# Performance work log

Measured on AMD Instinct MI355X. Metric: run time of the kernel, lower is better.

## Reference

```python
import jax, jax.numpy as jnp
import numpy as np

NUM_HEADS = 16


def setup_inputs() -> dict:
    key = jax.random.key(0)
    ks = jax.random.split(key, 3)
    B, S, E = 8, 1024, 1024
    x = jax.random.normal(ks[0], (B, S, E), dtype=jnp.float32)
    W_attn = jax.random.normal(ks[1], (E, 3 * E), dtype=jnp.float32) * (1.0 / np.sqrt(E))
    b_attn = jnp.zeros((3 * E,), dtype=jnp.float32)
    W_proj = jax.random.normal(ks[2], (E, E), dtype=jnp.float32) * (1.0 / np.sqrt(E))
    b_proj = jnp.zeros((E,), dtype=jnp.float32)
    return {"x": x, "W_attn": W_attn, "b_attn": b_attn, "W_proj": W_proj, "b_proj": b_proj}


def reference(x, W_attn, b_attn, W_proj, b_proj):
    # The module's blockwise "flash" loop implements exact causal softmax
    # attention (online softmax is mathematically identical); dropout is
    # inactive in eval mode.
    B, S, E = x.shape
    H = NUM_HEADS
    D = E // H
    qkv = x @ W_attn + b_attn  # [B,S,3E]
    q, k, v = jnp.split(qkv, 3, axis=-1)

    def split_heads(t):
        return t.reshape(B, S, H, D).transpose(0, 2, 1, 3)  # [B,H,S,D]

    q, k, v = split_heads(q), split_heads(k), split_heads(v)
    scores = jnp.einsum("bhqd,bhkd->bhqk", q, k) / jnp.sqrt(jnp.asarray(D, x.dtype))
    causal = jnp.tril(jnp.ones((S, S), dtype=bool))
    scores = jnp.where(causal, scores, -jnp.inf)
    probs = jax.nn.softmax(scores, axis=-1)
    out = jnp.einsum("bhqk,bhkd->bhqd", probs, v)  # [B,H,S,D]
    out = out.transpose(0, 2, 1, 3).reshape(B, S, E)
    return out @ W_proj + b_proj
```

## Files before the change

### kernel.cpp

```cpp
#include <hip/hip_runtime.h>
#include <hip/hip_bf16.h>
#include <stdint.h>

typedef unsigned short ushort_t;
typedef __attribute__((ext_vector_type(8))) __bf16 bf16x8;
typedef __attribute__((ext_vector_type(4))) float f32x4;

typedef const __attribute__((address_space(1))) uint32_t* gptr_t;
typedef __attribute__((address_space(3))) uint32_t* lptr_t;

__device__ __forceinline__ ushort_t f2bf(float f) {
  union { float f; uint32_t u; } x; x.f = f;
  uint32_t u = x.u;
  uint32_t r = (u + 0x7fffu + ((u >> 16) & 1u)) >> 16;
  return (ushort_t)r;
}

__device__ __forceinline__ uint32_t cvt_pk_bf16(float lo, float hi) {
  uint32_t r;
  asm("v_cvt_pk_bf16_f32 %0, %1, %2" : "=v"(r) : "v"(lo), "v"(hi));
  return r;
}

__device__ __forceinline__ void gload_lds16(const void* g, void* l) {
  __builtin_amdgcn_global_load_lds((gptr_t)g, (lptr_t)l, 16, 0, 0);
}

__global__ void cast_x(const float* __restrict__ in, ushort_t* __restrict__ out, int n) {
  const int idx = (blockIdx.x * 256 + threadIdx.x) * 4;
  if (idx < n) {
    const float4 v = *(const float4*)(in + idx);
    ushort4 o;
    o.x = f2bf(v.x); o.y = f2bf(v.y); o.z = f2bf(v.z); o.w = f2bf(v.w);
    *(ushort4*)(out + idx) = o;
  }
}

__global__ void transpose_cast(const float* __restrict__ in, ushort_t* __restrict__ out, int K, int N) {
  __shared__ ushort_t t[32][33];
  const int n0 = blockIdx.x * 32, k0 = blockIdx.y * 32;
  const int c = threadIdx.x & 31, r0 = threadIdx.x >> 5;
#pragma unroll
  for (int i = 0; i < 4; ++i) {
    const int r = r0 + i * 8;
    t[r][c] = f2bf(in[(size_t)(k0 + r) * N + n0 + c]);
  }
  __syncthreads();
#pragma unroll
  for (int i = 0; i < 4; ++i) {
    const int r = r0 + i * 8;
    out[(size_t)(n0 + r) * K + k0 + c] = t[c][r];
  }
}

template<int MODE>
__global__ __launch_bounds__(256, 4) void gemm_bt(
    const ushort_t* __restrict__ A, const ushort_t* __restrict__ Bt,
    const float* __restrict__ bias,
    ushort_t* __restrict__ Cq, ushort_t* __restrict__ Ck, ushort_t* __restrict__ Cv,
    float* __restrict__ Cf,
    int M, int N, int K, float qscale)
{
  __shared__ ushort_t As[128 * 64];
  __shared__ ushort_t Bs[128 * 64];
  const int tid = threadIdx.x;
  const int w = tid >> 6, l = tid & 63;
  const int bm = blockIdx.y * 128, bn = blockIdx.x * 128;
  const int lr = l >> 3, lp = l & 7;
  const int l16 = l & 15, lhi = l >> 4;
  const int wm = (w >> 1) * 64, wn = (w & 1) * 64;

  f32x4 acc[4][4] = {};

  for (int kt = 0; kt < K; kt += 64) {
#pragma unroll
    for (int i = 0; i < 4; ++i) {
      const int ci = i * 4 + w;
      const int row = ci * 8 + lr;
      const int sc = (lp ^ (row & 7)) * 8;
      gload_lds16(A + (size_t)(bm + row) * K + kt + sc, &As[ci * 512]);
      gload_lds16(Bt + (size_t)(bn + row) * K + kt + sc, &Bs[ci * 512]);
    }
    __syncthreads();

    bf16x8 af[4][2], bfr[4][2];
#pragma unroll
    for (int mf = 0; mf < 4; ++mf) {
      const int row = wm + mf * 16 + l16;
#pragma unroll
      for (int kf = 0; kf < 2; ++kf) {
        const int ch = (lhi + kf * 4) ^ (row & 7);
        af[mf][kf] = *(const bf16x8*)((const char*)&As[row * 64] + ch * 16);
      }
    }
#pragma unroll
    for (int nf = 0; nf < 4; ++nf) {
      const int row = wn + nf * 16 + l16;
#pragma unroll
      for (int kf = 0; kf < 2; ++kf) {
        const int ch = (lhi + kf * 4) ^ (row & 7);
        bfr[nf][kf] = *(const bf16x8*)((const char*)&Bs[row * 64] + ch * 16);
      }
    }
#pragma unroll
    for (int kf = 0; kf < 2; ++kf)
#pragma unroll
      for (int mf = 0; mf < 4; ++mf)
#pragma unroll
        for (int nf = 0; nf < 4; ++nf)
          acc[mf][nf] = __builtin_amdgcn_mfma_f32_16x16x32_bf16(
              af[mf][kf], bfr[nf][kf], acc[mf][nf], 0, 0, 0);
    __syncthreads();
  }

#pragma unroll
  for (int mf = 0; mf < 4; ++mf) {
#pragma unroll
    for (int nf = 0; nf < 4; ++nf) {
      const int col = bn + wn + nf * 16 + l16;
      const float bv = bias[col];
#pragma unroll
      for (int r = 0; r < 4; ++r) {
        const int row = bm + wm + mf * 16 + lhi * 4 + r;
        float v = acc[mf][nf][r] + bv;
        if constexpr (MODE == 1) {
          Cf[(size_t)row * N + col] = v;
        } else {
          const int region = col >> 10;
          const int hcol = col & 1023;
          const int b_ = row >> 10, s_ = row & 1023;
          const int h_ = hcol >> 6, d_ = hcol & 63;
          if (region == 2) {
            Cv[((size_t)(b_ * 16 + h_) * 64 + d_) * 1024 + s_] = f2bf(v);
          } else {
            ushort_t* base = (region == 0) ? Cq : Ck;
            if (region == 0) v *= qscale;
            base[((size_t)(b_ * 16 + h_) * 1024 + s_) * 64 + d_] = f2bf(v);
          }
        }
      }
    }
  }
}

__global__ __launch_bounds__(256, 2) void attn_kernel(
    const ushort_t* __restrict__ Q, const ushort_t* __restrict__ Kk,
    const ushort_t* __restrict__ Vt, ushort_t* __restrict__ O)
{
  __shared__ ushort_t Pl[8][32 * 68];
  const int tid = threadIdx.x;
  const int w = tid >> 6, l = tid & 63;
  const int l16 = l & 15, lhi = l >> 4;

  const int bid = blockIdx.x;
  const int bh = ((bid >> 5) << 3) | (bid & 7);
  const int p  = (bid >> 3) & 3;
  const int qtH = 7 - p, qtL = p;
  const int qbH = qtH * 128 + w * 32;
  const int qbL = qtL * 128 + w * 32;
  const int ntH = (qbH >> 6) + 1;
  const int ntL = (qbL >> 6) + 1;
  const size_t hb = (size_t)bh * (1024 * 64);
  const int b_ = bh >> 4, h_ = bh & 15;

  bf16x8 qfH[2][2], qfL[2][2];
#pragma unroll
  for (int mf = 0; mf < 2; ++mf)
#pragma unroll
    for (int kf = 0; kf < 2; ++kf) {
      qfH[mf][kf] = *(const bf16x8*)(Q + hb + (size_t)(qbH + mf * 16 + l16) * 64 + kf * 32 + lhi * 8);
      qfL[mf][kf] = *(const bf16x8*)(Q + hb + (size_t)(qbL + mf * 16 + l16) * 64 + kf * 32 + lhi * 8);
    }

  f32x4 oH[2][4] = {}, oL[2][4] = {};
  float mH[2] = {-1e30f, -1e30f}, lsH[2] = {0.0f, 0.0f};
  float mL[2] = {-1e30f, -1e30f}, lsL[2] = {0.0f, 0.0f};
  char* const pbH = (char*)&Pl[w * 2 + 0][0];
  char* const pbL = (char*)&Pl[w * 2 + 1][0];

  for (int t = 0; t < ntH; ++t) {
    const int kv0 = t * 64;

    bf16x8 kb[4][2], vb[4][2];
#pragma unroll
    for (int nf = 0; nf < 4; ++nf)
#pragma unroll
      for (int kf = 0; kf < 2; ++kf) {
        kb[nf][kf] = *(const bf16x8*)(Kk + hb + (size_t)(kv0 + nf * 16 + l16) * 64 + kf * 32 + lhi * 8);
        vb[nf][kf] = *(const bf16x8*)(Vt + hb + (size_t)(nf * 16 + l16) * 1024 + kv0 + kf * 32 + lhi * 8);
      }

    auto half = [&](const bf16x8 (&qf)[2][2], f32x4 (&o)[2][4],
                    float (&m_run)[2], float (&l_run)[2],
                    const int qbase, char* const pbase) {
      f32x4 s[2][4] = {};
#pragma unroll
      for (int nf = 0; nf < 4; ++nf)
#pragma unroll
        for (int kf = 0; kf < 2; ++kf)
#pragma unroll
          for (int mf = 0; mf < 2; ++mf)
            s[mf][nf] = __builtin_amdgcn_mfma_f32_16x16x32_bf16(kb[nf][kf], qf[mf][kf], s[mf][nf], 0, 0, 0);

      if (kv0 + 63 > qbase) {
#pragma unroll
        for (int mf = 0; mf < 2; ++mf) {
          const int q = qbase + mf * 16 + l16;
#pragma unroll
          for (int nf = 0; nf < 4; ++nf)
#pragma unroll
            for (int r = 0; r < 4; ++r) {
              const int kv = kv0 + nf * 16 + lhi * 4 + r;
              if (kv > q) s[mf][nf][r] = -1e30f;
            }
        }
      }

#pragma unroll
      for (int mf = 0; mf < 2; ++mf) {
        float lmax = -1e30f;
#pragma unroll
        for (int nf = 0; nf < 4; ++nf)
#pragma unroll
          for (int r = 0; r < 4; ++r) lmax = fmaxf(lmax, s[mf][nf][r]);
        lmax = fmaxf(lmax, __shfl_xor(lmax, 16));
        lmax = fmaxf(lmax, __shfl_xor(lmax, 32));
        const float mnew = fmaxf(m_run[mf], lmax);
        const float corr = exp2f(m_run[mf] - mnew);
        float psum = 0.0f;
#pragma unroll
        for (int nf = 0; nf < 4; ++nf)
#pragma unroll
          for (int r = 0; r < 4; ++r) {
            const float pv = exp2f(s[mf][nf][r] - mnew);
            s[mf][nf][r] = pv;
            psum += pv;
          }
        psum += __shfl_xor(psum, 16);
        psum += __shfl_xor(psum, 32);
        l_run[mf] = l_run[mf] * corr + psum;
        m_run[mf] = mnew;
#pragma unroll
        for (int nf = 0; nf < 4; ++nf) o[mf][nf] *= corr;

        const int q = mf * 16 + l16;
#pragma unroll
        for (int nf = 0; nf < 4; ++nf) {
          const uint32_t u0 = cvt_pk_bf16(s[mf][nf][0], s[mf][nf][1]);
          const uint32_t u1 = cvt_pk_bf16(s[mf][nf][2], s[mf][nf][3]);
          *(uint2*)(pbase + q * 136 + nf * 32 + lhi * 8) = make_uint2(u0, u1);
        }
      }

#pragma unroll
      for (int mf = 0; mf < 2; ++mf) {
        const int q = mf * 16 + l16;
#pragma unroll
        for (int kf = 0; kf < 2; ++kf) {
          const bf16x8 pb = *(const bf16x8*)(pbase + q * 136 + kf * 64 + lhi * 16);
#pragma unroll
          for (int nf = 0; nf < 4; ++nf)
            o[mf][nf] = __builtin_amdgcn_mfma_f32_16x16x32_bf16(vb[nf][kf], pb, o[mf][nf], 0, 0, 0);
        }
      }
    };

    half(qfH, oH, mH, lsH, qbH, pbH);
    if (t < ntL) half(qfL, oL, mL, lsL, qbL, pbL);
  }

  auto epi = [&](f32x4 (&o)[2][4], float (&l_run)[2], const int qbase) {
#pragma unroll
    for (int mf = 0; mf < 2; ++mf) {
      const float inv = 1.0f / l_run[mf];
      const int qrow = qbase + mf * 16 + l16;
      const size_t rb = ((size_t)(b_ * 1024 + qrow)) * 1024 + h_ * 64;
#pragma unroll
      for (int nf = 0; nf < 4; ++nf) {
        const uint32_t u0 = cvt_pk_bf16(o[mf][nf][0] * inv, o[mf][nf][1] * inv);
        const uint32_t u1 = cvt_pk_bf16(o[mf][nf][2] * inv, o[mf][nf][3] * inv);
        *(uint2*)(O + rb + nf * 16 + lhi * 4) = make_uint2(u0, u1);
      }
    }
  };
  epi(oH, lsH, qbH);
  epi(oL, lsL, qbL);
}

extern "C" void kernel_launch(void* const* d_in, const int* in_sizes, int n_in,
                              void* d_out, int out_size, void* d_ws, size_t ws_size,
                              hipStream_t stream) {
  const float* x      = (const float*)d_in[0];
  const float* W_attn = (const float*)d_in[1];
  const float* b_attn = (const float*)d_in[2];
  const float* W_proj = (const float*)d_in[3];
  const float* b_proj = (const float*)d_in[4];
  float* out = (float*)d_out;

  const int M = 8192;
  const int E = 1024, N3 = 3072;
  const size_t T = (size_t)M * E;

  char* p = (char*)d_ws;
  ushort_t* xb  = (ushort_t*)p; p += T * 2;
  ushort_t* Wab = (ushort_t*)p; p += (size_t)N3 * E * 2;
  ushort_t* Wpb = (ushort_t*)p; p += (size_t)E * E * 2;
  ushort_t* Qb  = (ushort_t*)p; p += T * 2;
  ushort_t* Kb  = (ushort_t*)p; p += T * 2;
  ushort_t* Vtb = (ushort_t*)p; p += T * 2;

  const float qscale = 0.125f * 1.4426950408889634f;

  cast_x<<<dim3((int)(T / 1024)), dim3(256), 0, stream>>>(x, xb, (int)T);
  transpose_cast<<<dim3(N3 / 32, E / 32), dim3(256), 0, stream>>>(W_attn, Wab, E, N3);
  transpose_cast<<<dim3(E / 32, E / 32), dim3(256), 0, stream>>>(W_proj, Wpb, E, E);
  gemm_bt<2><<<dim3(N3 / 128, M / 128), dim3(256), 0, stream>>>(
      xb, Wab, b_attn, Qb, Kb, Vtb, nullptr, M, N3, E, qscale);
  attn_kernel<<<dim3(512), dim3(256), 0, stream>>>(Qb, Kb, Vtb, xb);
  gemm_bt<1><<<dim3(E / 128, M / 128), dim3(256), 0, stream>>>(
      xb, Wpb, b_proj, nullptr, nullptr, nullptr, out, M, E, E, 1.0f);
}
```

Measured before the change: 191.3 us.

## Fuse prep kernels, add MFMA priority hints, and lazy softmax rescaling

```diff
diff --git a/kernel.cpp b/kernel.cpp
--- a/kernel.cpp
+++ b/kernel.cpp
@@ -26,30 +26,39 @@
   __builtin_amdgcn_global_load_lds((gptr_t)g, (lptr_t)l, 16, 0, 0);
 }
 
-__global__ void cast_x(const float* __restrict__ in, ushort_t* __restrict__ out, int n) {
-  const int idx = (blockIdx.x * 256 + threadIdx.x) * 4;
-  if (idx < n) {
-    const float4 v = *(const float4*)(in + idx);
+__global__ void prep(const float* __restrict__ x, ushort_t* __restrict__ xb,
+                     const float* __restrict__ Wa, ushort_t* __restrict__ Wab,
+                     const float* __restrict__ Wp, ushort_t* __restrict__ Wpb) {
+  const int bid = blockIdx.x;
+  if (bid < 8192) {
+    const int idx = (bid * 256 + threadIdx.x) * 4;
+    const float4 v = *(const float4*)(x + idx);
     ushort4 o;
     o.x = f2bf(v.x); o.y = f2bf(v.y); o.z = f2bf(v.z); o.w = f2bf(v.w);
-    *(ushort4*)(out + idx) = o;
-  }
-}
-
-__global__ void transpose_cast(const float* __restrict__ in, ushort_t* __restrict__ out, int K, int N) {
-  __shared__ ushort_t t[32][33];
-  const int n0 = blockIdx.x * 32, k0 = blockIdx.y * 32;
-  const int c = threadIdx.x & 31, r0 = threadIdx.x >> 5;
-#pragma unroll
-  for (int i = 0; i < 4; ++i) {
-    const int r = r0 + i * 8;
-    t[r][c] = f2bf(in[(size_t)(k0 + r) * N + n0 + c]);
-  }
-  __syncthreads();
-#pragma unroll
-  for (int i = 0; i < 4; ++i) {
-    const int r = r0 + i * 8;
-    out[(size_t)(n0 + r) * K + k0 + c] = t[c][r];
+    *(ushort4*)(xb + idx) = o;
+  } else {
+    __shared__ ushort_t t[32][33];
+    const float* in; ushort_t* out; int N, n0, k0;
+    const int K = 1024;
+    if (bid < 11264) {
+      const int i = bid - 8192; in = Wa; out = Wab; N = 3072;
+      n0 = (i % 96) * 32; k0 = (i / 96) * 32;
+    } else {
+      const int i = bid - 11264; in = Wp; out = Wpb; N = 1024;
+      n0 = (i % 32) * 32; k0 = (i / 32) * 32;
+    }
+    const int c = threadIdx.x & 31, r0 = threadIdx.x >> 5;
+#pragma unroll
+    for (int i = 0; i < 4; ++i) {
+      const int r = r0 + i * 8;
+      t[r][c] = f2bf(in[(size_t)(k0 + r) * N + n0 + c]);
+    }
+    __syncthreads();
+#pragma unroll
+    for (int i = 0; i < 4; ++i) {
+      const int r = r0 + i * 8;
+      out[(size_t)(n0 + r) * K + k0 + c] = t[c][r];
+    }
   }
 }
 
@@ -194,6 +203,7 @@
                     float (&m_run)[2], float (&l_run)[2],
                     const int qbase, char* const pbase) {
       f32x4 s[2][4] = {};
+      __builtin_amdgcn_s_setprio(1);
 #pragma unroll
       for (int nf = 0; nf < 4; ++nf)
 #pragma unroll
@@ -201,6 +211,7 @@
 #pragma unroll
           for (int mf = 0; mf < 2; ++mf)
             s[mf][nf] = __builtin_amdgcn_mfma_f32_16x16x32_bf16(kb[nf][kf], qf[mf][kf], s[mf][nf], 0, 0, 0);
+      __builtin_amdgcn_s_setprio(0);
 
       if (kv0 + 63 > qbase) {
 #pragma unroll
@@ -225,23 +236,38 @@
           for (int r = 0; r < 4; ++r) lmax = fmaxf(lmax, s[mf][nf][r]);
         lmax = fmaxf(lmax, __shfl_xor(lmax, 16));
         lmax = fmaxf(lmax, __shfl_xor(lmax, 32));
-        const float mnew = fmaxf(m_run[mf], lmax);
-        const float corr = exp2f(m_run[mf] - mnew);
+        const float mold = m_run[mf];
         float psum = 0.0f;
-#pragma unroll
-        for (int nf = 0; nf < 4; ++nf)
-#pragma unroll
-          for (int r = 0; r < 4; ++r) {
-            const float pv = exp2f(s[mf][nf][r] - mnew);
-            s[mf][nf][r] = pv;
-            psum += pv;
-          }
-        psum += __shfl_xor(psum, 16);
-        psum += __shfl_xor(psum, 32);
-        l_run[mf] = l_run[mf] * corr + psum;
-        m_run[mf] = mnew;
-#pragma unroll
-        for (int nf = 0; nf < 4; ++nf) o[mf][nf] *= corr;
+        if (__all(lmax - mold <= 8.0f)) {
+#pragma unroll
+          for (int nf = 0; nf < 4; ++nf)
+#pragma unroll
+            for (int r = 0; r < 4; ++r) {
+              const float pv = exp2f(s[mf][nf][r] - mold);
+              s[mf][nf][r] = pv;
+              psum += pv;
+            }
+          psum += __shfl_xor(psum, 16);
+          psum += __shfl_xor(psum, 32);
+          l_run[mf] += psum;
+        } else {
+          const float mnew = fmaxf(mold, lmax);
+          const float corr = exp2f(mold - mnew);
+#pragma unroll
+          for (int nf = 0; nf < 4; ++nf)
+#pragma unroll
+            for (int r = 0; r < 4; ++r) {
+              const float pv = exp2f(s[mf][nf][r] - mnew);
+              s[mf][nf][r] = pv;
+              psum += pv;
+            }
+          psum += __shfl_xor(psum, 16);
+          psum += __shfl_xor(psum, 32);
+          l_run[mf] = l_run[mf] * corr + psum;
+          m_run[mf] = mnew;
+#pragma unroll
+          for (int nf = 0; nf < 4; ++nf) o[mf][nf] *= corr;
+        }
 
         const int q = mf * 16 + l16;
 #pragma unroll
@@ -258,9 +284,11 @@
 #pragma unroll
         for (int kf = 0; kf < 2; ++kf) {
           const bf16x8 pb = *(const bf16x8*)(pbase + q * 136 + kf * 64 + lhi * 16);
+          __builtin_amdgcn_s_setprio(1);
 #pragma unroll
           for (int nf = 0; nf < 4; ++nf)
             o[mf][nf] = __builtin_amdgcn_mfma_f32_16x16x32_bf16(vb[nf][kf], pb, o[mf][nf], 0, 0, 0);
+          __builtin_amdgcn_s_setprio(0);
         }
       }
     };
@@ -311,9 +339,7 @@
 
   const float qscale = 0.125f * 1.4426950408889634f;
 
-  cast_x<<<dim3((int)(T / 1024)), dim3(256), 0, stream>>>(x, xb, (int)T);
-  transpose_cast<<<dim3(N3 / 32, E / 32), dim3(256), 0, stream>>>(W_attn, Wab, E, N3);
-  transpose_cast<<<dim3(E / 32, E / 32), dim3(256), 0, stream>>>(W_proj, Wpb, E, E);
+  prep<<<dim3(12288), dim3(256), 0, stream>>>(x, xb, W_attn, Wab, W_proj, Wpb);
   gemm_bt<2><<<dim3(N3 / 128, M / 128), dim3(256), 0, stream>>>(
       xb, Wab, b_attn, Qb, Kb, Vtb, nullptr, M, N3, E, qscale);
   attn_kernel<<<dim3(512), dim3(256), 0, stream>>>(Qb, Kb, Vtb, xb);
```

Result: slower. 207.6 us (+8.5%).
